# Optimization experiments

Measured on AMD Instinct MI355X. Metric: run time of the kernel, lower is better.

Reference implementation:

```python
import jax, jax.numpy as jnp
import numpy as np

N_NODES = 100000
N_EDGES = 1600000
D = 64
NUM_HOPS = 3


def setup_inputs() -> dict:
    key = jax.random.key(0)
    ks = jax.random.split(key, 8)
    return {
        "H_l": jax.random.normal(ks[0], (N_NODES, D), dtype=jnp.float32),
        "edge_row": jax.random.randint(ks[1], (N_EDGES,), 0, N_NODES, dtype=jnp.int64),
        "edge_col": jax.random.randint(ks[2], (N_EDGES,), 0, N_NODES, dtype=jnp.int64),
        "edge_val": jax.random.uniform(ks[3], (N_EDGES,), dtype=jnp.float32),
        "out_degree": jax.random.uniform(ks[4], (N_NODES,), dtype=jnp.float32),
        "in_degree": jax.random.uniform(ks[5], (N_NODES,), dtype=jnp.float32),
        "hop_attention": jnp.ones((NUM_HOPS,), dtype=jnp.float32),
        "theta_out": jnp.full((NUM_HOPS,), 0.5, dtype=jnp.float32),
        "theta_in": jnp.full((NUM_HOPS,), 0.5, dtype=jnp.float32),
        "Theta": jax.random.normal(ks[6], (D, D), dtype=jnp.float32) * (6.0 ** 0.5) / (2 * D) ** 0.5,
    }


def reference(H_l, edge_row, edge_col, edge_val, out_degree, in_degree,
              hop_attention, theta_out, theta_in, Theta):
    n = H_l.shape[0]
    num_hops = hop_attention.shape[0]
    alpha = jax.nn.softmax(hop_attention)

    def spmm(rows, cols, X):
        # (A @ X)[r] = sum over edges (r,c): val * X[c]
        return jax.ops.segment_sum(edge_val[:, None] * X[cols], rows, num_segments=n)

    # fixed degree-scaled features (degrees clamped as in __init__)
    X_out = jnp.maximum(out_degree, 1e-8)[:, None] * H_l
    X_in = jnp.maximum(in_degree, 1e-8)[:, None] * H_l
    sum_term = jnp.zeros_like(H_l)
    for k in range(num_hops):
        # A^{k+1} @ (D_out H) computed by one more application of A per hop
        X_out = spmm(edge_row, edge_col, X_out)
        # (A^{k+1})^T @ (D_in H): transpose swaps row/col roles
        X_in = spmm(edge_col, edge_row, X_in)
        sum_term = sum_term + alpha[k] * (theta_out[k] * X_out + theta_in[k] * X_in)

    conv_term = jax.nn.sigmoid(sum_term @ Theta)
    return conv_term + H_l
```

## Files before the change

### kernel.cpp

```cpp
#include <hip/hip_runtime.h>
#include <hip/hip_fp16.h>

#define DFEAT 64
#define BKT_SHIFT 8
#define BKT_NODES 256
#define NBMAX 512
#define CH 4096
#define SRC_BITS 18
#define SRC_MASK ((1 << SRC_BITS) - 1)

__device__ __forceinline__ unsigned short f2h(float f) {
    return __half_as_ushort(__float2half(f));
}
__device__ __forceinline__ float h2f(unsigned short u) {
    return __half2float(__ushort_as_half(u));
}

__global__ void init_kernel(const float* __restrict__ H,
                            const float* __restrict__ outdeg,
                            const float* __restrict__ indeg,
                            const float* __restrict__ hop_att,
                            const float* __restrict__ th_out,
                            const float* __restrict__ th_in,
                            unsigned short* __restrict__ XAout,
                            unsigned short* __restrict__ XAin,
                            float* __restrict__ coefs, int n4) {
    int idx = blockIdx.x * blockDim.x + threadIdx.x;
    if (idx == 0) {
        float m = fmaxf(fmaxf(hop_att[0], hop_att[1]), hop_att[2]);
        float e0 = __expf(hop_att[0] - m);
        float e1 = __expf(hop_att[1] - m);
        float e2 = __expf(hop_att[2] - m);
        float inv = 1.0f / (e0 + e1 + e2);
        coefs[0] = e0 * inv * th_out[0]; coefs[1] = e0 * inv * th_in[0];
        coefs[2] = e1 * inv * th_out[1]; coefs[3] = e1 * inv * th_in[1];
        coefs[4] = e2 * inv * th_out[2]; coefs[5] = e2 * inv * th_in[2];
    }
    if (idx >= n4) return;
    int row = idx >> 4;
    float4 h = reinterpret_cast<const float4*>(H)[idx];
    float doo = fmaxf(outdeg[row], 1e-8f);
    float dii = fmaxf(indeg[row], 1e-8f);
    reinterpret_cast<ushort4*>(XAout)[idx] =
        make_ushort4(f2h(h.x * doo), f2h(h.y * doo), f2h(h.z * doo), f2h(h.w * doo));
    reinterpret_cast<ushort4*>(XAin)[idx] =
        make_ushort4(f2h(h.x * dii), f2h(h.y * dii), f2h(h.z * dii), f2h(h.w * dii));
}

__global__ __launch_bounds__(256) void hist2d_kernel(
        const int* __restrict__ erow, const int* __restrict__ ecol,
        int* __restrict__ cnt2, int nEdges, int nB, int nBlkA) {
    __shared__ int hR[NBMAX], hC[NBMAX];
    int k = blockIdx.x;
    for (int i = threadIdx.x; i < nB; i += 256) { hR[i] = 0; hC[i] = 0; }
    __syncthreads();
    int base = k * CH;
    int nV = min(CH, nEdges - base);
    for (int i = threadIdx.x; i < nV; i += 256) {
        atomicAdd(&hR[erow[base + i] >> BKT_SHIFT], 1);
        atomicAdd(&hC[ecol[base + i] >> BKT_SHIFT], 1);
    }
    __syncthreads();
    for (int b = threadIdx.x; b < nB; b += 256) {
        cnt2[(size_t)b * nBlkA + k] = hR[b];
        cnt2[((size_t)nB + b) * nBlkA + k] = hC[b];
    }
}

__global__ void scan_reduce1(const int* __restrict__ p, int* __restrict__ bsum,
                             int n) {
    int t = threadIdx.x, lane = t & 63, wid = t >> 6;
    int base = blockIdx.x * 1024 + t * 4;
    int s = 0;
#pragma unroll
    for (int i = 0; i < 4; ++i) { int idx = base + i; if (idx < n) s += p[idx]; }
#pragma unroll
    for (int o = 32; o >= 1; o >>= 1) s += __shfl_down(s, o, 64);
    __shared__ int wsum[4];
    if (lane == 0) wsum[wid] = s;
    __syncthreads();
    if (t == 0) bsum[blockIdx.x] = wsum[0] + wsum[1] + wsum[2] + wsum[3];
}

__global__ void scan_spine1(int* __restrict__ bsum, int nChunks) {
    int lane = threadIdx.x;
    int carry = 0;
    for (int base = 0; base < nChunks; base += 64) {
        int i = base + lane;
        int v = (i < nChunks) ? bsum[i] : 0;
        int s = v;
#pragma unroll
        for (int o = 1; o < 64; o <<= 1) {
            int x = __shfl_up(s, o, 64);
            if (lane >= o) s += x;
        }
        if (i < nChunks) bsum[i] = carry + s - v;
        carry += __shfl(s, 63, 64);
    }
}

__global__ void scan_down1(int* __restrict__ p, const int* __restrict__ bsum,
                           int n) {
    int t = threadIdx.x, lane = t & 63, wid = t >> 6;
    int base = blockIdx.x * 1024 + t * 4;
    int v[4];
    int tsum = 0;
#pragma unroll
    for (int i = 0; i < 4; ++i) {
        v[i] = (base + i < n) ? p[base + i] : 0;
        tsum += v[i];
    }
    int inc = tsum;
#pragma unroll
    for (int o = 1; o < 64; o <<= 1) {
        int x = __shfl_up(inc, o, 64);
        if (lane >= o) inc += x;
    }
    __shared__ int wsum[4];
    if (lane == 63) wsum[wid] = inc;
    __syncthreads();
    int woff = 0;
    for (int w = 0; w < wid; ++w) woff += wsum[w];
    int run = bsum[blockIdx.x] + woff + inc - tsum;
#pragma unroll
    for (int i = 0; i < 4; ++i) {
        if (base + i < n) p[base + i] = run;
        run += v[i];
    }
}

__global__ __launch_bounds__(256) void partA_kernel(
        const int* __restrict__ erow, const int* __restrict__ ecol,
        const float* __restrict__ eval, const int* __restrict__ base2,
        int2* __restrict__ recR, int2* __restrict__ recC,
        int nEdges, int nB, int nBlkA) {
    __shared__ int hist[NBMAX], scn[NBMAX], cur[NBMAX], gbase[NBMAX];
    __shared__ unsigned short keybuf[CH], slotKey[CH];
    __shared__ int2 stage[CH];
    int dir = blockIdx.y;
    const int* dk = dir ? ecol : erow;
    const int* ds = dir ? erow : ecol;
    int2* rec = dir ? recC : recR;
    int k = blockIdx.x;
    int base = k * CH;
    int nV = min(CH, nEdges - base);
    for (int i = threadIdx.x; i < nB; i += 256) {
        hist[i] = 0; cur[i] = 0;
        gbase[i] = base2[((size_t)dir * nB + i) * nBlkA + k] - dir * nEdges;
    }
    __syncthreads();
    for (int i = threadIdx.x; i < nV; i += 256) {
        int key = dk[base + i] >> BKT_SHIFT;
        keybuf[i] = (unsigned short)key;
        atomicAdd(&hist[key], 1);
    }
    __syncthreads();
    if (threadIdx.x < 64) {
        int lane = threadIdx.x;
        int carry = 0;
        for (int bb = 0; bb < nB; bb += 64) {
            int i = bb + lane;
            int v = (i < nB) ? hist[i] : 0;
            int s = v;
#pragma unroll
            for (int o = 1; o < 64; o <<= 1) {
                int x = __shfl_up(s, o, 64);
                if (lane >= o) s += x;
            }
            if (i < nB) scn[i] = carry + s - v;
            carry += __shfl(s, 63, 64);
        }
    }
    __syncthreads();
    for (int i = threadIdx.x; i < nV; i += 256) {
        int e = base + i;
        int key = keybuf[i];
        int slot = scn[key] + atomicAdd(&cur[key], 1);
        int dl = dk[e] & (BKT_NODES - 1);
        stage[slot] = make_int2(ds[e] | (dl << SRC_BITS), __float_as_int(eval[e]));
        slotKey[slot] = (unsigned short)key;
    }
    __syncthreads();
    for (int i = threadIdx.x; i < nV; i += 256) {
        int key = slotKey[i];
        rec[gbase[key] + (i - scn[key])] = stage[i];
    }
}

__global__ __launch_bounds__(256) void partB_kernel(
        const int2* __restrict__ recR, const int2* __restrict__ recC,
        const int* __restrict__ base2,
        int* __restrict__ rowptr, int* __restrict__ colptr,
        unsigned* __restrict__ pairsR, unsigned* __restrict__ pairsC,
        int nEdges, int nB, int nBlkA, int nNodes) {
    __shared__ int hist[BKT_NODES], scn[BKT_NODES], cur[BKT_NODES];
    int dir = blockIdx.y;
    int b = blockIdx.x;
    const int2* rec = dir ? recC : recR;
    unsigned* pairs = dir ? pairsC : pairsR;
    int* nptr = dir ? colptr : rowptr;
    int segB = base2[((size_t)dir * nB + b) * nBlkA] - dir * nEdges;
    int segE = (b == nB - 1) ? nEdges
             : base2[((size_t)dir * nB + b + 1) * nBlkA] - dir * nEdges;
    int t = threadIdx.x;
    hist[t] = 0; cur[t] = 0;
    __syncthreads();
    for (int j = segB + t; j < segE; j += 256)
        atomicAdd(&hist[(rec[j].x >> SRC_BITS) & (BKT_NODES - 1)], 1);
    __syncthreads();
    if (t < 64) {
        int lane = t, carry = 0;
        for (int bb = 0; bb < BKT_NODES; bb += 64) {
            int i = bb + lane;
            int v = hist[i], s = v;
#pragma unroll
            for (int o = 1; o < 64; o <<= 1) {
                int x = __shfl_up(s, o, 64);
                if (lane >= o) s += x;
            }
            scn[i] = carry + s - v;
            carry += __shfl(s, 63, 64);
        }
    }
    __syncthreads();
    int node = (b << BKT_SHIFT) + t;
    if (node < nNodes) nptr[node] = segB + scn[t];
    if (b == nB - 1 && t == 0) nptr[nNodes] = nEdges;
    for (int j = segB + t; j < segE; j += 256) {
        int2 r = rec[j];
        int dl = (r.x >> SRC_BITS) & (BKT_NODES - 1);
        int slot = segB + scn[dl] + atomicAdd(&cur[dl], 1);
        unsigned vh = f2h(__int_as_float(r.y)) & 0x7FFFu;
        pairs[slot] = ((unsigned)(r.x & SRC_MASK) << 15) | vh;
    }
}

__device__ __forceinline__ void gather_rows(
        const int* __restrict__ ptr, const unsigned* __restrict__ pairs,
        const __half* __restrict__ X, int node, int hb, int sub,
        float& axo, float& ayo) {
    float2 a0{0.f,0.f}, a1{0.f,0.f}, a2{0.f,0.f}, a3{0.f,0.f};
    float2 a4{0.f,0.f}, a5{0.f,0.f}, a6{0.f,0.f}, a7{0.f,0.f};
    int j = ptr[node], eE = ptr[node + 1];
    auto step = [&](int jj, float2& a) {
        unsigned p = pairs[jj + hb];
        float2 x = __half22float2(*(const __half2*)(X + (p >> 15) * DFEAT + 2 * sub));
        float v = h2f(p & 0x7FFFu);
        a.x += v * x.x; a.y += v * x.y;
    };
    for (; j + 16 <= eE; j += 16) {
        step(j, a0);      step(j + 2, a1);  step(j + 4, a2);  step(j + 6, a3);
        step(j + 8, a4);  step(j + 10, a5); step(j + 12, a6); step(j + 14, a7);
    }
    if (j + 8 <= eE) {
        step(j, a0); step(j + 2, a1); step(j + 4, a2); step(j + 6, a3);
        j += 8;
    }
#pragma unroll
    for (int q = 0; q < 4; ++q) {
        int idx = j + 2 * q + hb;
        unsigned p = (idx < eE) ? pairs[idx] : 0u;
        float2 x = __half22float2(*(const __half2*)(X + (p >> 15) * DFEAT + 2 * sub));
        float v = h2f(p & 0x7FFFu);
        a4.x += v * x.x; a4.y += v * x.y;
    }
    float ax = ((a0.x + a1.x) + (a2.x + a3.x)) + ((a4.x + a5.x) + (a6.x + a7.x));
    float ay = ((a0.y + a1.y) + (a2.y + a3.y)) + ((a4.y + a5.y) + (a6.y + a7.y));
    ax += __shfl_xor(ax, 32, 64);
    ay += __shfl_xor(ay, 32, 64);
    axo = ax; ayo = ay;
}

template <int FIRST>
__global__ __launch_bounds__(256) void spmm_split(
        const int* __restrict__ rowptr, const unsigned* __restrict__ pairsR,
        const int* __restrict__ colptr, const unsigned* __restrict__ pairsC,
        const __half* __restrict__ Xout, const __half* __restrict__ Xin,
        unsigned short* __restrict__ Yout, unsigned short* __restrict__ Yin,
        unsigned short* __restrict__ sumO, unsigned short* __restrict__ sumI,
        const float* __restrict__ coefs, int k, int nNodes) {
    int b = blockIdx.x;
    int slot = b & 7;
    int dir = slot >> 2;
    int g = (b >> 3) * 4 + (slot & 3);
    int wid = threadIdx.x >> 6;
    int lane = threadIdx.x & 63;
    int node = g * 4 + wid;
    if (node >= nNodes) return;

    const int* ptr = dir ? colptr : rowptr;
    const unsigned* pairs = dir ? pairsC : pairsR;
    const __half* X = dir ? Xin : Xout;
    unsigned short* Y = dir ? Yin : Yout;
    unsigned short* sm = dir ? sumI : sumO;
    float cf = coefs[2 * k + dir];

    int hb = lane >> 5;
    int sub = lane & 31;

    float ax, ay;
    gather_rows(ptr, pairs, X, node, hb, sub, ax, ay);

    if (hb == 0) {
        int off = node * DFEAT + 2 * sub;
        __half2 yv = __floats2half2_rn(ax, ay);
        __builtin_nontemporal_store(*reinterpret_cast<unsigned*>(&yv),
                                    reinterpret_cast<unsigned*>(Y + off));
        float sx = cf * ax, sy = cf * ay;
        if (!FIRST) {
            __half2 old = *reinterpret_cast<const __half2*>(sm + off);
            float2 of = __half22float2(old);
            sx += of.x; sy += of.y;
        }
        __half2 sv = __floats2half2_rn(sx, sy);
        __builtin_nontemporal_store(*reinterpret_cast<unsigned*>(&sv),
                                    reinterpret_cast<unsigned*>(sm + off));
    }
}

__global__ __launch_bounds__(256) void spmm_last(
        const int* __restrict__ rowptr, const unsigned* __restrict__ pairsR,
        const int* __restrict__ colptr, const unsigned* __restrict__ pairsC,
        const __half* __restrict__ Xout, const __half* __restrict__ Xin,
        const unsigned short* __restrict__ sumO,
        const unsigned short* __restrict__ sumI,
        const float* __restrict__ H, const float* __restrict__ Theta,
        float* __restrict__ out, const float* __restrict__ coefs,
        int k, int nNodes) {
    __shared__ float Th[64 * 64];
    __shared__ float Srow[4 * 64];
    int wid = threadIdx.x >> 6;
    int lane = threadIdx.x & 63;
    int node = blockIdx.x * 4 + wid;
    bool live = node < nNodes;
    int nodeC = live ? node : 0;

    for (int i = threadIdx.x; i < 64 * 64; i += 256) Th[i] = Theta[i];

    float co = coefs[2 * k], ci = coefs[2 * k + 1];
    int hb = lane >> 5;
    int sub = lane & 31;

    float axO, ayO, axI, ayI;
    gather_rows(rowptr, pairsR, Xout, nodeC, hb, sub, axO, ayO);
    gather_rows(colptr, pairsC, Xin,  nodeC, hb, sub, axI, ayI);

    int off = nodeC * DFEAT + 2 * sub;
    float s0 = h2f(sumO[off])     + h2f(sumI[off])     + co * axO + ci * axI;
    float s1 = h2f(sumO[off + 1]) + h2f(sumI[off + 1]) + co * ayO + ci * ayI;

    __syncthreads();
    if (hb == 0) {
        Srow[wid * 64 + 2 * sub]     = s0;
        Srow[wid * 64 + 2 * sub + 1] = s1;
    }
    float acc = 0.f;
#pragma unroll
    for (int kk = 0; kk < 64; ++kk)
        acc += Srow[wid * 64 + kk] * Th[kk * 64 + lane];
    if (live) {
        float r = 1.0f / (1.0f + __expf(-acc)) + H[nodeC * DFEAT + lane];
        __builtin_nontemporal_store(r, &out[nodeC * DFEAT + lane]);
    }
}

extern "C" void kernel_launch(void* const* d_in, const int* in_sizes, int n_in,
                              void* d_out, int out_size, void* d_ws, size_t ws_size,
                              hipStream_t stream) {
    const float* H      = (const float*)d_in[0];
    const int*   erow   = (const int*)d_in[1];
    const int*   ecol   = (const int*)d_in[2];
    const float* eval   = (const float*)d_in[3];
    const float* outdeg = (const float*)d_in[4];
    const float* indeg  = (const float*)d_in[5];
    const float* hopatt = (const float*)d_in[6];
    const float* thout  = (const float*)d_in[7];
    const float* thin   = (const float*)d_in[8];
    const float* Theta  = (const float*)d_in[9];
    float* out = (float*)d_out;

    int nNodes = in_sizes[0] / DFEAT;
    int nEdges = in_sizes[1];

    char* ws = (char*)d_ws;
    size_t off = 0;
    auto alloc = [&](size_t bytes) {
        void* p = ws + off;
        off += (bytes + 255) & ~(size_t)255;
        return p;
    };
    size_t xBytes = (size_t)nNodes * DFEAT * sizeof(unsigned short);
    unsigned short* XAout = (unsigned short*)alloc(xBytes);
    unsigned short* XAin  = (unsigned short*)alloc(xBytes);
    unsigned short* XBout = (unsigned short*)alloc(xBytes);
    unsigned short* XBin  = (unsigned short*)alloc(xBytes);
    unsigned short* sumO  = (unsigned short*)alloc(xBytes);
    unsigned short* sumI  = (unsigned short*)alloc(xBytes);
    int*   rowptr = (int*)alloc((size_t)(nNodes + 1) * sizeof(int));
    int*   colptr = (int*)alloc((size_t)(nNodes + 1) * sizeof(int));
    int2*  recR   = (int2*)alloc((size_t)nEdges * sizeof(int2));
    int2*  recC   = (int2*)alloc((size_t)nEdges * sizeof(int2));
    unsigned* pairsR = (unsigned*)alloc((size_t)nEdges * sizeof(unsigned));
    unsigned* pairsC = (unsigned*)alloc((size_t)nEdges * sizeof(unsigned));

    int nB    = (nNodes + BKT_NODES - 1) >> BKT_SHIFT;
    int nBlkA = (nEdges + CH - 1) / CH;
    int L = 2 * nB * nBlkA;
    int nChunks = (L + 1023) / 1024;
    int*   cnt2 = (int*)alloc((size_t)L * sizeof(int));
    int*   bsum = (int*)alloc((size_t)nChunks * sizeof(int));
    float* coefs = (float*)alloc(8 * sizeof(float));

    int n4 = nNodes * (DFEAT / 4);
    int ewBlocks = (n4 + 255) / 256;
    int gPerDir = (nNodes + 3) / 4;
    int grid8 = (gPerDir + 3) / 4;
    int splitGrid = 8 * grid8;
    int nodeBlocks = (nNodes + 3) / 4;

    init_kernel<<<ewBlocks, 256, 0, stream>>>(H, outdeg, indeg, hopatt, thout, thin,
                                              XAout, XAin, coefs, n4);
    hist2d_kernel<<<nBlkA, 256, 0, stream>>>(erow, ecol, cnt2, nEdges, nB, nBlkA);
    scan_reduce1<<<nChunks, 256, 0, stream>>>(cnt2, bsum, L);
    scan_spine1<<<1, 64, 0, stream>>>(bsum, nChunks);
    scan_down1<<<nChunks, 256, 0, stream>>>(cnt2, bsum, L);
    partA_kernel<<<dim3(nBlkA, 2), 256, 0, stream>>>(erow, ecol, eval, cnt2,
                                                     recR, recC, nEdges, nB, nBlkA);
    partB_kernel<<<dim3(nB, 2), 256, 0, stream>>>(recR, recC, cnt2,
                                                  rowptr, colptr, pairsR, pairsC,
                                                  nEdges, nB, nBlkA, nNodes);

    spmm_split<1><<<splitGrid, 256, 0, stream>>>(rowptr, pairsR, colptr, pairsC,
                                                 (const __half*)XAout, (const __half*)XAin,
                                                 XBout, XBin, sumO, sumI,
                                                 coefs, 0, nNodes);
    spmm_split<0><<<splitGrid, 256, 0, stream>>>(rowptr, pairsR, colptr, pairsC,
                                                 (const __half*)XBout, (const __half*)XBin,
                                                 XAout, XAin, sumO, sumI,
                                                 coefs, 1, nNodes);

    spmm_last<<<nodeBlocks, 256, 0, stream>>>(rowptr, pairsR, colptr, pairsC,
                                              (const __half*)XAout, (const __half*)XAin,
                                              sumO, sumI, H, Theta, out,
                                              coefs, 2, nNodes);
}
```

Before: 412.1 us.

## Split edge records into key/half arrays and move last hop to split SpMM plus GEMM

The partition records go from int2 (src|local, float val) to separate 32-bit key and fp16 value arrays. This cuts bucket-scatter traffic and pre-converts values to half in partA. The third hop now runs through the split SpMM kernel without writing Y, and a separate final kernel tiles 32 rows per block for the Theta GEMM, sigmoid and residual. This adds a launch and a round trip through the fp16 sum buffers. SRC_BITS drops to 17, which still covers 100k nodes but limits node count to 131072.

```diff
diff --git a/kernel.cpp b/kernel.cpp
--- a/kernel.cpp
+++ b/kernel.cpp
@@ -6,7 +6,7 @@
 #define BKT_NODES 256
 #define NBMAX 512
 #define CH 4096
-#define SRC_BITS 18
+#define SRC_BITS 17
 #define SRC_MASK ((1 << SRC_BITS) - 1)
 
 __device__ __forceinline__ unsigned short f2h(float f) {
@@ -132,15 +132,18 @@
 __global__ __launch_bounds__(256) void partA_kernel(
         const int* __restrict__ erow, const int* __restrict__ ecol,
         const float* __restrict__ eval, const int* __restrict__ base2,
-        int2* __restrict__ recR, int2* __restrict__ recC,
+        unsigned* __restrict__ recRkey, unsigned short* __restrict__ recRval,
+        unsigned* __restrict__ recCkey, unsigned short* __restrict__ recCval,
         int nEdges, int nB, int nBlkA) {
     __shared__ int hist[NBMAX], scn[NBMAX], cur[NBMAX], gbase[NBMAX];
     __shared__ unsigned short keybuf[CH], slotKey[CH];
-    __shared__ int2 stage[CH];
+    __shared__ unsigned stageK[CH];
+    __shared__ unsigned short stageV[CH];
     int dir = blockIdx.y;
     const int* dk = dir ? ecol : erow;
     const int* ds = dir ? erow : ecol;
-    int2* rec = dir ? recC : recR;
+    unsigned* recK = dir ? recCkey : recRkey;
+    unsigned short* recV = dir ? recCval : recRval;
     int k = blockIdx.x;
     int base = k * CH;
     int nV = min(CH, nEdges - base);
@@ -177,18 +180,22 @@
         int key = keybuf[i];
         int slot = scn[key] + atomicAdd(&cur[key], 1);
         int dl = dk[e] & (BKT_NODES - 1);
-        stage[slot] = make_int2(ds[e] | (dl << SRC_BITS), __float_as_int(eval[e]));
+        stageK[slot] = (unsigned)ds[e] | ((unsigned)dl << SRC_BITS);
+        stageV[slot] = f2h(eval[e]);
         slotKey[slot] = (unsigned short)key;
     }
     __syncthreads();
     for (int i = threadIdx.x; i < nV; i += 256) {
         int key = slotKey[i];
-        rec[gbase[key] + (i - scn[key])] = stage[i];
+        int o = gbase[key] + (i - scn[key]);
+        recK[o] = stageK[i];
+        recV[o] = stageV[i];
     }
 }
 
 __global__ __launch_bounds__(256) void partB_kernel(
-        const int2* __restrict__ recR, const int2* __restrict__ recC,
+        const unsigned* __restrict__ recRkey, const unsigned short* __restrict__ recRval,
+        const unsigned* __restrict__ recCkey, const unsigned short* __restrict__ recCval,
         const int* __restrict__ base2,
         int* __restrict__ rowptr, int* __restrict__ colptr,
         unsigned* __restrict__ pairsR, unsigned* __restrict__ pairsC,
@@ -196,7 +203,8 @@
     __shared__ int hist[BKT_NODES], scn[BKT_NODES], cur[BKT_NODES];
     int dir = blockIdx.y;
     int b = blockIdx.x;
-    const int2* rec = dir ? recC : recR;
+    const unsigned* recK = dir ? recCkey : recRkey;
+    const unsigned short* recV = dir ? recCval : recRval;
     unsigned* pairs = dir ? pairsC : pairsR;
     int* nptr = dir ? colptr : rowptr;
     int segB = base2[((size_t)dir * nB + b) * nBlkA] - dir * nEdges;
@@ -206,7 +214,7 @@
     hist[t] = 0; cur[t] = 0;
     __syncthreads();
     for (int j = segB + t; j < segE; j += 256)
-        atomicAdd(&hist[(rec[j].x >> SRC_BITS) & (BKT_NODES - 1)], 1);
+        atomicAdd(&hist[(recK[j] >> SRC_BITS) & (BKT_NODES - 1)], 1);
     __syncthreads();
     if (t < 64) {
         int lane = t, carry = 0;
@@ -227,11 +235,10 @@
     if (node < nNodes) nptr[node] = segB + scn[t];
     if (b == nB - 1 && t == 0) nptr[nNodes] = nEdges;
     for (int j = segB + t; j < segE; j += 256) {
-        int2 r = rec[j];
-        int dl = (r.x >> SRC_BITS) & (BKT_NODES - 1);
+        unsigned key = recK[j];
+        int dl = (key >> SRC_BITS) & (BKT_NODES - 1);
         int slot = segB + scn[dl] + atomicAdd(&cur[dl], 1);
-        unsigned vh = f2h(__int_as_float(r.y)) & 0x7FFFu;
-        pairs[slot] = ((unsigned)(r.x & SRC_MASK) << 15) | vh;
+        pairs[slot] = ((key & SRC_MASK) << 15) | (recV[j] & 0x7FFFu);
     }
 }
 
@@ -271,7 +278,7 @@
     axo = ax; ayo = ay;
 }
 
-template <int FIRST>
+template <int FIRST, int WRITEY>
 __global__ __launch_bounds__(256) void spmm_split(
         const int* __restrict__ rowptr, const unsigned* __restrict__ pairsR,
         const int* __restrict__ colptr, const unsigned* __restrict__ pairsC,
@@ -303,9 +310,11 @@
 
     if (hb == 0) {
         int off = node * DFEAT + 2 * sub;
-        __half2 yv = __floats2half2_rn(ax, ay);
-        __builtin_nontemporal_store(*reinterpret_cast<unsigned*>(&yv),
-                                    reinterpret_cast<unsigned*>(Y + off));
+        if (WRITEY) {
+            __half2 yv = __floats2half2_rn(ax, ay);
+            __builtin_nontemporal_store(*reinterpret_cast<unsigned*>(&yv),
+                                        reinterpret_cast<unsigned*>(Y + off));
+        }
         float sx = cf * ax, sy = cf * ay;
         if (!FIRST) {
             __half2 old = *reinterpret_cast<const __half2*>(sm + off);
@@ -318,49 +327,39 @@
     }
 }
 
-__global__ __launch_bounds__(256) void spmm_last(
-        const int* __restrict__ rowptr, const unsigned* __restrict__ pairsR,
-        const int* __restrict__ colptr, const unsigned* __restrict__ pairsC,
-        const __half* __restrict__ Xout, const __half* __restrict__ Xin,
+__global__ __launch_bounds__(256) void final_kernel(
         const unsigned short* __restrict__ sumO,
         const unsigned short* __restrict__ sumI,
         const float* __restrict__ H, const float* __restrict__ Theta,
-        float* __restrict__ out, const float* __restrict__ coefs,
-        int k, int nNodes) {
+        float* __restrict__ out, int nRows) {
     __shared__ float Th[64 * 64];
-    __shared__ float Srow[4 * 64];
-    int wid = threadIdx.x >> 6;
-    int lane = threadIdx.x & 63;
-    int node = blockIdx.x * 4 + wid;
-    bool live = node < nNodes;
-    int nodeC = live ? node : 0;
-
-    for (int i = threadIdx.x; i < 64 * 64; i += 256) Th[i] = Theta[i];
-
-    float co = coefs[2 * k], ci = coefs[2 * k + 1];
-    int hb = lane >> 5;
-    int sub = lane & 31;
-
-    float axO, ayO, axI, ayI;
-    gather_rows(rowptr, pairsR, Xout, nodeC, hb, sub, axO, ayO);
-    gather_rows(colptr, pairsC, Xin,  nodeC, hb, sub, axI, ayI);
-
-    int off = nodeC * DFEAT + 2 * sub;
-    float s0 = h2f(sumO[off])     + h2f(sumI[off])     + co * axO + ci * axI;
-    float s1 = h2f(sumO[off + 1]) + h2f(sumI[off + 1]) + co * ayO + ci * ayI;
-
-    __syncthreads();
-    if (hb == 0) {
-        Srow[wid * 64 + 2 * sub]     = s0;
-        Srow[wid * 64 + 2 * sub + 1] = s1;
-    }
-    float acc = 0.f;
-#pragma unroll
-    for (int kk = 0; kk < 64; ++kk)
-        acc += Srow[wid * 64 + kk] * Th[kk * 64 + lane];
-    if (live) {
-        float r = 1.0f / (1.0f + __expf(-acc)) + H[nodeC * DFEAT + lane];
-        __builtin_nontemporal_store(r, &out[nodeC * DFEAT + lane]);
+    __shared__ float S[32 * 64];
+    int t = threadIdx.x;
+    for (int i = t; i < 64 * 64; i += 256) Th[i] = Theta[i];
+    int rbase = blockIdx.x * 32;
+    for (int i = t; i < 32 * 64; i += 256) {
+        int r = rbase + (i >> 6);
+        float v = 0.f;
+        if (r < nRows) {
+            int off = r * DFEAT + (i & 63);
+            v = h2f(sumO[off]) + h2f(sumI[off]);
+        }
+        S[i] = v;
+    }
+    __syncthreads();
+    int c = t & 63;
+#pragma unroll
+    for (int rr = 0; rr < 8; ++rr) {
+        int rl = (t >> 6) + rr * 4;
+        int row = rbase + rl;
+        float acc = 0.f;
+#pragma unroll
+        for (int kk = 0; kk < 64; ++kk)
+            acc += S[rl * 64 + kk] * Th[kk * 64 + c];
+        if (row < nRows) {
+            float r = 1.0f / (1.0f + __expf(-acc)) + H[row * DFEAT + c];
+            __builtin_nontemporal_store(r, &out[row * DFEAT + c]);
+        }
     }
 }
 
@@ -398,8 +397,10 @@
     unsigned short* sumI  = (unsigned short*)alloc(xBytes);
     int*   rowptr = (int*)alloc((size_t)(nNodes + 1) * sizeof(int));
     int*   colptr = (int*)alloc((size_t)(nNodes + 1) * sizeof(int));
-    int2*  recR   = (int2*)alloc((size_t)nEdges * sizeof(int2));
-    int2*  recC   = (int2*)alloc((size_t)nEdges * sizeof(int2));
+    unsigned*       recRkey = (unsigned*)alloc((size_t)nEdges * sizeof(unsigned));
+    unsigned short* recRval = (unsigned short*)alloc((size_t)nEdges * sizeof(unsigned short));
+    unsigned*       recCkey = (unsigned*)alloc((size_t)nEdges * sizeof(unsigned));
+    unsigned short* recCval = (unsigned short*)alloc((size_t)nEdges * sizeof(unsigned short));
     unsigned* pairsR = (unsigned*)alloc((size_t)nEdges * sizeof(unsigned));
     unsigned* pairsC = (unsigned*)alloc((size_t)nEdges * sizeof(unsigned));
 
@@ -416,7 +417,6 @@
     int gPerDir = (nNodes + 3) / 4;
     int grid8 = (gPerDir + 3) / 4;
     int splitGrid = 8 * grid8;
-    int nodeBlocks = (nNodes + 3) / 4;
 
     init_kernel<<<ewBlocks, 256, 0, stream>>>(H, outdeg, indeg, hopatt, thout, thin,
                                               XAout, XAin, coefs, n4);
@@ -425,22 +425,25 @@
     scan_spine1<<<1, 64, 0, stream>>>(bsum, nChunks);
     scan_down1<<<nChunks, 256, 0, stream>>>(cnt2, bsum, L);
     partA_kernel<<<dim3(nBlkA, 2), 256, 0, stream>>>(erow, ecol, eval, cnt2,
-                                                     recR, recC, nEdges, nB, nBlkA);
-    partB_kernel<<<dim3(nB, 2), 256, 0, stream>>>(recR, recC, cnt2,
-                                                  rowptr, colptr, pairsR, pairsC,
+                                                     recRkey, recRval, recCkey, recCval,
+                                                     nEdges, nB, nBlkA);
+    partB_kernel<<<dim3(nB, 2), 256, 0, stream>>>(recRkey, recRval, recCkey, recCval,
+                                                  cnt2, rowptr, colptr, pairsR, pairsC,
                                                   nEdges, nB, nBlkA, nNodes);
 
-    spmm_split<1><<<splitGrid, 256, 0, stream>>>(rowptr, pairsR, colptr, pairsC,
-                                                 (const __half*)XAout, (const __half*)XAin,
-                                                 XBout, XBin, sumO, sumI,
-                                                 coefs, 0, nNodes);
-    spmm_split<0><<<splitGrid, 256, 0, stream>>>(rowptr, pairsR, colptr, pairsC,
-                                                 (const __half*)XBout, (const __half*)XBin,
-                                                 XAout, XAin, sumO, sumI,
-                                                 coefs, 1, nNodes);
-
-    spmm_last<<<nodeBlocks, 256, 0, stream>>>(rowptr, pairsR, colptr, pairsC,
-                                              (const __half*)XAout, (const __half*)XAin,
-                                              sumO, sumI, H, Theta, out,
-                                              coefs, 2, nNodes);
-}
+    spmm_split<1, 1><<<splitGrid, 256, 0, stream>>>(rowptr, pairsR, colptr, pairsC,
+                                                    (const __half*)XAout, (const __half*)XAin,
+                                                    XBout, XBin, sumO, sumI,
+                                                    coefs, 0, nNodes);
+    spmm_split<0, 1><<<splitGrid, 256, 0, stream>>>(rowptr, pairsR, colptr, pairsC,
+                                                    (const __half*)XBout, (const __half*)XBin,
+                                                    XAout, XAin, sumO, sumI,
+                                                    coefs, 1, nNodes);
+    spmm_split<0, 0><<<splitGrid, 256, 0, stream>>>(rowptr, pairsR, colptr, pairsC,
+                                                    (const __half*)XAout, (const __half*)XAin,
+                                                    nullptr, nullptr, sumO, sumI,
+                                                    coefs, 2, nNodes);
+
+    final_kernel<<<(nNodes + 31) / 32, 256, 0, stream>>>(sumO, sumI, H, Theta,
+                                                         out, nNodes);
+}
```

Result: slower. 433.8 us (+5.3%).
